# Kernel optimization log

Measured on AMD Instinct MI355X. Metric: run time of the kernel, lower is better.

The kernel has to match this reference:

```python
import jax, jax.numpy as jnp
import numpy as np

# Directable[TL_table[i]] for i = 0..7: (dx, dy) with dx=horizontal shift, dy=vertical shift
# dx=+1 -> shift right (zero-fill col 0), dx=-1 -> shift left; dy=+1 -> shift down, dy=-1 -> shift up.
DIRS = [(1, 1), (0, 1), (-1, 1), (1, 0), (-1, 0), (1, -1), (0, -1), (-1, -1)]


def _shift(img, dx, dy):
    # img: [B, H, W]; zero-padded shift equivalent to bmm with the sparse translation matrices
    if dx == 1:
        img = jnp.pad(img[..., :-1], ((0, 0), (0, 0), (1, 0)))
    elif dx == -1:
        img = jnp.pad(img[..., 1:], ((0, 0), (0, 0), (0, 1)))
    if dy == 1:
        img = jnp.pad(img[:, :-1, :], ((0, 0), (1, 0), (0, 0)))
    elif dy == -1:
        img = jnp.pad(img[:, 1:, :], ((0, 0), (0, 1), (0, 0)))
    return img


def _bce(p, t):
    # torch F.binary_cross_entropy clamps log terms at -100
    logp = jnp.maximum(jnp.log(p), -100.0)
    log1mp = jnp.maximum(jnp.log(1.0 - p), -100.0)
    return -jnp.mean(t * logp + (1.0 - t) * log1mp)


def setup_inputs() -> dict:
    key = jax.random.key(0)
    k1, k2, k3 = jax.random.split(key, 3)
    B, C, H, W = 16, 8, 512, 512
    c_map = jax.random.normal(k1, (B, C, H, W), dtype=jnp.float32)
    target = jax.random.randint(k2, (B, 1, H, W), 0, 2, dtype=jnp.int32)
    con_target = jax.random.randint(k3, (B, C, H, W), 0, 2, dtype=jnp.int32)
    return {"c_map": c_map, "target": target, "con_target": con_target}


def reference(c_map, target, con_target):
    target = target.astype(jnp.float32)        # [B,1,H,W]
    con_target = con_target.astype(jnp.float32)  # [B,8,H,W]

    p = jax.nn.sigmoid(c_map)  # [B,8,H,W]

    # Bilateral voting: shifted[i] = shift(p[:, 7-i]) in direction DIRS[i]
    shifted = jnp.stack(
        [_shift(p[:, 7 - i], dx, dy) for i, (dx, dy) in enumerate(DIRS)], axis=1
    )  # [B,8,H,W]
    vote_out = p * shifted                       # [B,8,H,W] (== bimap.squeeze(1))
    final_pred = jnp.max(vote_out, axis=1, keepdims=True)  # [B,1,H,W]

    # dice loss (sums over dims (1,2) of the 4D tensors, as in the original)
    smooth = 0.001
    i_sum = jnp.sum(target, axis=(1, 2))
    j_sum = jnp.sum(final_pred, axis=(1, 2))
    inter = jnp.sum(target * final_pred, axis=(1, 2))
    loss_dice = jnp.mean(1.0 - (2.0 * inter + smooth) / (i_sum + j_sum + smooth))

    # edge (decouple) loss
    sum_conn = jnp.sum(con_target, axis=1)  # [B,H,W]
    edge = ((sum_conn < 8) & (sum_conn > 0)).astype(p.dtype)
    pred_min = jnp.min(vote_out, axis=1) * edge
    decouple_loss = _bce(pred_min, jnp.zeros_like(pred_min))

    bce_loss = _bce(final_pred, target)
    conmap_l = _bce(p, con_target)
    bimap_l = _bce(vote_out, con_target)

    return 0.8 * conmap_l + decouple_loss + 0.2 * bimap_l + bce_loss + loss_dice
```

## Files before the change

kernel.cpp:

```cpp
#include <hip/hip_runtime.h>

namespace {
constexpr int Bn = 16, Hn = 512, Wn = 512;
constexpr int HW  = Hn * Wn;
constexpr int CHW = 8 * HW;
constexpr int NCOL = Bn * Wn;
constexpr int WALK = 2;
constexpr int GX   = Hn / (2 * WALK);
constexpr int NBLK = GX * Bn;
constexpr int FBLK = 32;

constexpr float L2E  = 1.4426950408889634f;
constexpr float LN2  = 0.6931471805599453f;
constexpr float CLMP = -144.26950408889634f;

__device__ __forceinline__ float frcp(float x) { return __builtin_amdgcn_rcpf(x); }
#if __has_builtin(__builtin_amdgcn_exp2f)
__device__ __forceinline__ float fexp2(float x) { return __builtin_amdgcn_exp2f(x); }
#else
__device__ __forceinline__ float fexp2(float x) { return exp2f(x); }
#endif
#if __has_builtin(__builtin_amdgcn_logf)
__device__ __forceinline__ float flog2(float x) { return __builtin_amdgcn_logf(x); }
#else
__device__ __forceinline__ float flog2(float x) { return log2f(x); }
#endif
}


__global__ __launch_bounds__(256) void bicon_main(
    const float* __restrict__ c_map,
    const int*   __restrict__ target,
    const int*   __restrict__ con_target,
    float* __restrict__ col_i, float* __restrict__ col_j, float* __restrict__ col_x,
    double* __restrict__ bscal)
{
    const int tid  = threadIdx.x;
    const int lane = tid & 63;
    const int wv   = tid >> 6;
    const int half = wv & 1;
    const int rg   = wv >> 1;
    const int b    = blockIdx.y;
    const int hstart = blockIdx.x * (2 * WALK) + rg * WALK;
    const int wq   = half * 256 + lane * 4;

    const float* cm = c_map      + (size_t)b * CHW;
    const int*   ct = con_target + (size_t)b * CHW;
    const int*   tg = target     + (size_t)b * HW;

    float s_con = 0.f, s_bi = 0.f, s_bce = 0.f, s_dec = 0.f;
    float ci[4] = {0, 0, 0, 0}, cj[4] = {0, 0, 0, 0}, cx[4] = {0, 0, 0, 0};

    auto sig4 = [&](const float4& v, float s[4]) {
        s[0] = frcp(1.f + fexp2(-v.x * L2E));
        s[1] = frcp(1.f + fexp2(-v.y * L2E));
        s[2] = frcp(1.f + fexp2(-v.z * L2E));
        s[3] = frcp(1.f + fexp2(-v.w * L2E));
    };

    float C0[4], C1[4], C2[4], P5[4], P6[4], P7[4];
    {
        const int pb = hstart * Wn + wq;
        sig4(*(const float4*)(cm + 0 * HW + pb), C0);
        sig4(*(const float4*)(cm + 1 * HW + pb), C1);
        sig4(*(const float4*)(cm + 2 * HW + pb), C2);
    }
    if (hstart > 0) {
        const int pb = (hstart - 1) * Wn + wq;
        sig4(*(const float4*)(cm + 5 * HW + pb), P5);
        sig4(*(const float4*)(cm + 6 * HW + pb), P6);
        sig4(*(const float4*)(cm + 7 * HW + pb), P7);
    } else {
#pragma unroll
        for (int k = 0; k < 4; ++k) { P5[k] = 0.f; P6[k] = 0.f; P7[k] = 0.f; }
    }

    const bool edR = (wq + 4 == Wn);
    const bool edL = (wq == 0);

    int h = hstart;
#pragma unroll 1
    for (int r = 0; r < WALK; ++r, ++h) {
        const int  base  = h * Wn + wq;
        const bool hasDn = (h + 1 < Hn);
        const bool hasUp = (h > 0);

        const float4 xa3 = *(const float4*)(cm + 3 * HW + base);
        const float4 xa4 = *(const float4*)(cm + 4 * HW + base);
        const float4 xa5 = *(const float4*)(cm + 5 * HW + base);
        const float4 xa6 = *(const float4*)(cm + 6 * HW + base);
        const float4 xa7 = *(const float4*)(cm + 7 * HW + base);
        const float4 xf0 = *(const float4*)(cm + 0 * HW + base + Wn);
        const float4 xf1 = *(const float4*)(cm + 1 * HW + base + Wn);
        const float4 xf2 = *(const float4*)(cm + 2 * HW + base + Wn);
        const float bx0 = cm[0 * HW + base + Wn + 4];
        const float bx2 = cm[2 * HW + base + Wn - 1];
        const float bx3 = cm[3 * HW + base + 4];
        const float bx4 = cm[4 * HW + base - 1];
        const float bx5 = cm[5 * HW + base - Wn + 4];
        const float bx7 = cm[7 * HW + base - Wn - 1];
        const int4  t4  = *(const int4*)(tg + base);

        unsigned lo = 0u;
#pragma unroll
        for (int c = 0; c < 8; ++c) {
            const int4 u = *(const int4*)(ct + c * HW + base);
            lo |= ((unsigned)u.x << c)        | ((unsigned)u.y << (8 + c)) |
                  ((unsigned)u.z << (16 + c)) | ((unsigned)u.w << (24 + c));
        }

        float dp[4] = {1.f, 1.f, 1.f, 1.f};
        float ys[4] = {0.f, 0.f, 0.f, 0.f};
        float c3[4], c4[4], c5[4], c6[4], c7[4];
        auto fresh = [&](int c, const float4& v, float s[4]) {
            const float xs[4] = {v.x, v.y, v.z, v.w};
#pragma unroll
            for (int k = 0; k < 4; ++k) {
                const float y = xs[k] * L2E;
                const float e = fexp2(-y);
                const float d = 1.f + e;
                s[k] = frcp(d);
                dp[k] *= d;
                ys[k] += ((lo >> (8 * k + c)) & 1u) ? 0.f : y;
            }
        };
        fresh(3, xa3, c3); fresh(4, xa4, c4); fresh(5, xa5, c5);
        fresh(6, xa6, c6); fresh(7, xa7, c7);

#pragma unroll
        for (int k = 0; k < 4; ++k) {
            const float q0 = ((lo >> (8 * k + 0)) & 1u) ? C0[k] : 1.f - C0[k];
            const float q1 = ((lo >> (8 * k + 1)) & 1u) ? C1[k] : 1.f - C1[k];
            const float q2 = ((lo >> (8 * k + 2)) & 1u) ? C2[k] : 1.f - C2[k];
            s_con += flog2(q0 * q1 * q2) - flog2(dp[k]) - ys[k];
        }

        float F0[4], F1[4], F2[4];
        sig4(xf0, F0); sig4(xf1, F1); sig4(xf2, F2);
        const float s0b = frcp(1.f + fexp2(-bx0 * L2E));
        const float s2b = frcp(1.f + fexp2(-bx2 * L2E));
        const float s3b = frcp(1.f + fexp2(-bx3 * L2E));
        const float s4b = frcp(1.f + fexp2(-bx4 * L2E));
        const float s5b = frcp(1.f + fexp2(-bx5 * L2E));
        const float s7b = frcp(1.f + fexp2(-bx7 * L2E));

        float n0[4], n1[4], n2[4], n3[4], n4[4], n5[4], n6[4], n7[4];
#pragma unroll
        for (int k = 0; k < 3; ++k) {
            n0[k] = F0[k + 1]; n3[k] = c3[k + 1]; n5[k] = P5[k + 1];
            n2[k + 1] = F2[k]; n4[k + 1] = c4[k]; n7[k + 1] = P7[k];
        }
        n0[3] = edR ? 0.f : s0b;  n3[3] = edR ? 0.f : s3b;  n5[3] = edR ? 0.f : s5b;
        n2[0] = edL ? 0.f : s2b;  n4[0] = edL ? 0.f : s4b;  n7[0] = edL ? 0.f : s7b;
#pragma unroll
        for (int k = 0; k < 4; ++k) {
            n1[k] = hasDn ? F1[k] : 0.f;
            n6[k] = hasUp ? P6[k] : 0.f;
            if (!hasDn) { n0[k] = 0.f; n2[k] = 0.f; }
            if (!hasUp) { n5[k] = 0.f; n7[k] = 0.f; }
        }

        float vmax[4] = {0.f, 0.f, 0.f, 0.f}, vmin[4] = {2.f, 2.f, 2.f, 2.f};
        float pr[4]   = {1.f, 1.f, 1.f, 1.f};
        float zc[4]   = {0.f, 0.f, 0.f, 0.f};
        auto vote = [&](int i, const float p[4], const float n[4]) {
#pragma unroll
            for (int k = 0; k < 4; ++k) {
                const float v = p[k] * n[k];
                vmax[k] = fmaxf(vmax[k], v);
                vmin[k] = fminf(vmin[k], v);
                const bool bit = (lo >> (8 * k + i)) & 1u;
                const bool z   = bit && (v == 0.f);
                float sel = bit ? v : 1.f - v;
                sel = z ? 1.f : sel;
                zc[k] += z ? 1.f : 0.f;
                pr[k] *= sel;
            }
        };
        vote(0, C0, n7); vote(1, C1, n6); vote(2, C2, n5); vote(3, c3, n4);
#pragma unroll
        for (int k = 0; k < 4; ++k) { s_bi += flog2(pr[k]); pr[k] = 1.f; }
        vote(4, c4, n3); vote(5, c5, n2); vote(6, c6, n1); vote(7, c7, n0);
#pragma unroll
        for (int k = 0; k < 4; ++k) { s_bi += flog2(pr[k]) + CLMP * zc[k]; }

        const int tk[4] = {t4.x, t4.y, t4.z, t4.w};
#pragma unroll
        for (int k = 0; k < 4; ++k) {
            const float fm = vmax[k];
            s_bce += fmaxf(flog2(tk[k] ? fm : 1.f - fm), CLMP);
            const int sc = __popc((int)((lo >> (8 * k)) & 0xffu));
            s_dec += (sc > 0 && sc < 8) ? fmaxf(flog2(1.f - vmin[k]), CLMP) : 0.f;
            ci[k] += (float)tk[k];
            cj[k] += fm;
            cx[k] += tk[k] ? fm : 0.f;
        }

#pragma unroll
        for (int k = 0; k < 4; ++k) {
            C0[k] = F0[k]; C1[k] = F1[k]; C2[k] = F2[k];
            P5[k] = c5[k]; P6[k] = c6[k]; P7[k] = c7[k];
        }
    }

    __shared__ float cred[3][4][256];
#pragma unroll
    for (int k = 0; k < 4; ++k) {
        cred[0][wv][(lane << 2) + k] = ci[k];
        cred[1][wv][(lane << 2) + k] = cj[k];
        cred[2][wv][(lane << 2) + k] = cx[k];
    }

#pragma unroll
    for (int off = 32; off > 0; off >>= 1) {
        s_con += __shfl_down(s_con, off);
        s_bi  += __shfl_down(s_bi,  off);
        s_bce += __shfl_down(s_bce, off);
        s_dec += __shfl_down(s_dec, off);
    }
    __shared__ float wred[4][4];
    if (lane == 0) {
        wred[wv][0] = s_con * LN2; wred[wv][1] = s_bi * LN2;
        wred[wv][2] = s_bce * LN2; wred[wv][3] = s_dec * LN2;
    }
    __syncthreads();

#pragma unroll
    for (int j = tid; j < 512; j += 256) {
        const int hj = j >> 8, cidx = j & 255;
        atomicAdd(&col_i[b * Wn + j], cred[0][hj][cidx] + cred[0][hj + 2][cidx]);
        atomicAdd(&col_j[b * Wn + j], cred[1][hj][cidx] + cred[1][hj + 2][cidx]);
        atomicAdd(&col_x[b * Wn + j], cred[2][hj][cidx] + cred[2][hj + 2][cidx]);
    }
    if (tid < 4) {
        bscal[((size_t)blockIdx.y * GX + blockIdx.x) * 4 + tid] =
            (double)(wred[0][tid] + wred[1][tid] + wred[2][tid] + wred[3][tid]);
    }
}

__global__ __launch_bounds__(256) void bicon_finish(
    const float* __restrict__ col_i,
    const float* __restrict__ col_j,
    const float* __restrict__ col_x,
    const double* __restrict__ bscal,
    float* __restrict__ out)
{
    const int tid = threadIdx.x;
    const int col = blockIdx.x * 256 + tid;

    double part;
    {
        const float fi = col_i[col], fj = col_j[col], fx = col_x[col];
        part = (1.0 - (2.0 * (double)fx + 0.001) /
                      ((double)fi + (double)fj + 0.001)) / 8192.0;
    }
    if (tid < 64) {
        const int s = blockIdx.x * 64 + tid;
        const double c0 = bscal[s * 4 + 0], c1 = bscal[s * 4 + 1];
        const double c2 = bscal[s * 4 + 2], c3 = bscal[s * 4 + 3];
        part += -0.8 * c0 / 33554432.0 - 0.2 * c1 / 33554432.0
                - c2 / 4194304.0 - c3 / 4194304.0;
    }
#pragma unroll
    for (int off = 32; off > 0; off >>= 1) part += __shfl_down(part, off);
    __shared__ double red[4];
    if ((tid & 63) == 0) red[tid >> 6] = part;
    __syncthreads();
    if (tid == 0) atomicAdd(out, (float)(red[0] + red[1] + red[2] + red[3]));
}

extern "C" void kernel_launch(void* const* d_in, const int* in_sizes, int n_in,
                              void* d_out, int out_size, void* d_ws, size_t ws_size,
                              hipStream_t stream) {
    const float* c_map      = (const float*)d_in[0];
    const int*   target     = (const int*)d_in[1];
    const int*   con_target = (const int*)d_in[2];
    float* out = (float*)d_out;

    char* ws = (char*)d_ws;
    float*  col_i = (float*)ws;
    float*  col_j = col_i + NCOL;
    float*  col_x = col_j + NCOL;
    double* bscal = (double*)(ws + 3 * NCOL * sizeof(float));

    hipMemsetAsync(d_ws, 0, 3 * NCOL * sizeof(float), stream);
    hipMemsetAsync(d_out, 0, sizeof(float), stream);

    dim3 grid(GX, Bn);
    dim3 block(256);
    bicon_main<<<grid, block, 0, stream>>>(c_map, target, con_target,
                                           col_i, col_j, col_x, bscal);
    bicon_finish<<<FBLK, 256, 0, stream>>>(col_i, col_j, col_x, bscal, out);
}
```

Before: 303.5 us.

## Write per-block column partials to slabs instead of global atomics

```diff
diff --git a/kernel.cpp b/kernel.cpp
--- a/kernel.cpp
+++ b/kernel.cpp
@@ -8,7 +8,9 @@
 constexpr int WALK = 2;
 constexpr int GX   = Hn / (2 * WALK);
 constexpr int NBLK = GX * Bn;
-constexpr int FBLK = 32;
+constexpr int SLABN = NBLK * 512;
+constexpr int FBLK  = 32;
+constexpr int FBLK2 = 256;
 
 constexpr float L2E  = 1.4426950408889634f;
 constexpr float LN2  = 0.6931471805599453f;
@@ -28,7 +30,8 @@
 }
 
 
-__global__ __launch_bounds__(256) void bicon_main(
+template <bool SLAB>
+__global__ __launch_bounds__(256, 8) void bicon_main(
     const float* __restrict__ c_map,
     const int*   __restrict__ target,
     const int*   __restrict__ con_target,
@@ -225,17 +228,78 @@
     }
     __syncthreads();
 
-#pragma unroll
-    for (int j = tid; j < 512; j += 256) {
-        const int hj = j >> 8, cidx = j & 255;
-        atomicAdd(&col_i[b * Wn + j], cred[0][hj][cidx] + cred[0][hj + 2][cidx]);
-        atomicAdd(&col_j[b * Wn + j], cred[1][hj][cidx] + cred[1][hj + 2][cidx]);
-        atomicAdd(&col_x[b * Wn + j], cred[2][hj][cidx] + cred[2][hj + 2][cidx]);
+    if constexpr (SLAB) {
+        const size_t sb = ((size_t)(b * GX + blockIdx.x)) << 9;
+#pragma unroll
+        for (int j = tid; j < 512; j += 256) {
+            const int hj = j >> 8, cidx = j & 255;
+            col_i[sb + j] = cred[0][hj][cidx] + cred[0][hj + 2][cidx];
+            col_j[sb + j] = cred[1][hj][cidx] + cred[1][hj + 2][cidx];
+            col_x[sb + j] = cred[2][hj][cidx] + cred[2][hj + 2][cidx];
+        }
+    } else {
+#pragma unroll
+        for (int j = tid; j < 512; j += 256) {
+            const int hj = j >> 8, cidx = j & 255;
+            atomicAdd(&col_i[b * Wn + j], cred[0][hj][cidx] + cred[0][hj + 2][cidx]);
+            atomicAdd(&col_j[b * Wn + j], cred[1][hj][cidx] + cred[1][hj + 2][cidx]);
+            atomicAdd(&col_x[b * Wn + j], cred[2][hj][cidx] + cred[2][hj + 2][cidx]);
+        }
     }
     if (tid < 4) {
         bscal[((size_t)blockIdx.y * GX + blockIdx.x) * 4 + tid] =
             (double)(wred[0][tid] + wred[1][tid] + wred[2][tid] + wred[3][tid]);
     }
+}
+
+__global__ __launch_bounds__(256) void bicon_finish_slab(
+    const float* __restrict__ pI,
+    const float* __restrict__ pJ,
+    const float* __restrict__ pX,
+    const double* __restrict__ bscal,
+    float* __restrict__ out)
+{
+    const int tid = threadIdx.x;
+    const int w32 = tid & 31;
+    const int p   = tid >> 5;
+    const int col = blockIdx.x * 32 + w32;
+    const int b   = col >> 9;
+    const int w   = col & 511;
+
+    float fi = 0.f, fj = 0.f, fx = 0.f;
+    const size_t base = (((size_t)(b * GX + p * 16)) << 9) + w;
+#pragma unroll
+    for (int g = 0; g < 16; ++g) {
+        const size_t idx = base + ((size_t)g << 9);
+        fi += pI[idx]; fj += pJ[idx]; fx += pX[idx];
+    }
+    __shared__ float red[3][8][32];
+    red[0][p][w32] = fi; red[1][p][w32] = fj; red[2][p][w32] = fx;
+    __syncthreads();
+
+    double part = 0.0;
+    if (tid < 32) {
+        float si = 0.f, sj = 0.f, sx = 0.f;
+#pragma unroll
+        for (int q = 0; q < 8; ++q) {
+            si += red[0][q][tid]; sj += red[1][q][tid]; sx += red[2][q][tid];
+        }
+        part = (1.0 - (2.0 * (double)sx + 0.001) /
+                      ((double)si + (double)sj + 0.001)) / 8192.0;
+    }
+    if (tid >= 64 && tid < 72) {
+        const int s = blockIdx.x * 8 + (tid - 64);
+        const double c0 = bscal[s * 4 + 0], c1 = bscal[s * 4 + 1];
+        const double c2 = bscal[s * 4 + 2], c3 = bscal[s * 4 + 3];
+        part += -0.8 * c0 / 33554432.0 - 0.2 * c1 / 33554432.0
+                - c2 / 4194304.0 - c3 / 4194304.0;
+    }
+#pragma unroll
+    for (int off = 32; off > 0; off >>= 1) part += __shfl_down(part, off);
+    __shared__ double red2[4];
+    if ((tid & 63) == 0) red2[tid >> 6] = part;
+    __syncthreads();
+    if (tid == 0) atomicAdd(out, (float)(red2[0] + red2[1] + red2[2] + red2[3]));
 }
 
 __global__ __launch_bounds__(256) void bicon_finish(
@@ -278,17 +342,30 @@
     float* out = (float*)d_out;
 
     char* ws = (char*)d_ws;
-    float*  col_i = (float*)ws;
-    float*  col_j = col_i + NCOL;
-    float*  col_x = col_j + NCOL;
-    double* bscal = (double*)(ws + 3 * NCOL * sizeof(float));
-
-    hipMemsetAsync(d_ws, 0, 3 * NCOL * sizeof(float), stream);
-    hipMemsetAsync(d_out, 0, sizeof(float), stream);
+    const size_t slab_need = (size_t)3 * SLABN * sizeof(float)
+                           + (size_t)NBLK * 4 * sizeof(double);
 
     dim3 grid(GX, Bn);
     dim3 block(256);
-    bicon_main<<<grid, block, 0, stream>>>(c_map, target, con_target,
-                                           col_i, col_j, col_x, bscal);
-    bicon_finish<<<FBLK, 256, 0, stream>>>(col_i, col_j, col_x, bscal, out);
-}
+
+    hipMemsetAsync(d_out, 0, sizeof(float), stream);
+
+    if (ws_size >= slab_need) {
+        float*  pI    = (float*)ws;
+        float*  pJ    = pI + SLABN;
+        float*  pX    = pJ + SLABN;
+        double* bscal = (double*)(ws + (size_t)3 * SLABN * sizeof(float));
+        bicon_main<true><<<grid, block, 0, stream>>>(c_map, target, con_target,
+                                                     pI, pJ, pX, bscal);
+        bicon_finish_slab<<<FBLK2, 256, 0, stream>>>(pI, pJ, pX, bscal, out);
+    } else {
+        float*  col_i = (float*)ws;
+        float*  col_j = col_i + NCOL;
+        float*  col_x = col_j + NCOL;
+        double* bscal = (double*)(ws + 3 * NCOL * sizeof(float));
+        hipMemsetAsync(d_ws, 0, 3 * NCOL * sizeof(float), stream);
+        bicon_main<false><<<grid, block, 0, stream>>>(c_map, target, con_target,
+                                                      col_i, col_j, col_x, bscal);
+        bicon_finish<<<FBLK, 256, 0, stream>>>(col_i, col_j, col_x, bscal, out);
+    }
+}
```

Result: slower. 419.7 us (+38.3%).
